# Performance work log

Measured on AMD Instinct MI355X. Metric: run time of the kernel, lower is better.

Reference implementation:

```python
import jax, jax.numpy as jnp
import numpy as np

EPS = 1e-5
NEG_SLOPE = 0.01  # torch LeakyReLU default

def setup_inputs() -> dict:
    N, D, T, H = 4096, 64, 60, 128
    key = jax.random.key(0)
    ks = jax.random.split(key, 12)
    s_ih = 1.0 / np.sqrt(H)
    return {
        "x": jax.random.normal(ks[0], (N, D, T), dtype=jnp.float32),
        "bn1_gamma": jnp.ones((D,), jnp.float32),
        "bn1_beta": jnp.zeros((D,), jnp.float32),
        "W_ih": jax.random.uniform(ks[1], (4 * H, D), jnp.float32, -s_ih, s_ih),
        "W_hh": jax.random.uniform(ks[2], (4 * H, H), jnp.float32, -s_ih, s_ih),
        "b_ih": jax.random.uniform(ks[3], (4 * H,), jnp.float32, -s_ih, s_ih),
        "b_hh": jax.random.uniform(ks[4], (4 * H,), jnp.float32, -s_ih, s_ih),
        "bn2_gamma": jnp.ones((H,), jnp.float32),
        "bn2_beta": jnp.zeros((H,), jnp.float32),
        "W_t": jax.random.uniform(ks[5], (H, H), jnp.float32, -s_ih, s_ih),
        "b_t": jax.random.uniform(ks[6], (H,), jnp.float32, -s_ih, s_ih),
        "a": jax.random.normal(ks[7], (2 * H, 1), dtype=jnp.float32),
        "W_fc": jax.random.uniform(ks[8], (H, H), jnp.float32, -s_ih, s_ih),
        "b_fc": jax.random.uniform(ks[9], (H,), jnp.float32, -s_ih, s_ih),
        "W_out": jax.random.uniform(ks[10], (1, H), jnp.float32, -s_ih, s_ih),
        "b_out": jax.random.uniform(ks[11], (1,), jnp.float32, -s_ih, s_ih),
    }

def _leaky(z):
    return jnp.where(z >= 0, z, NEG_SLOPE * z)

def _lstm_last(x, W_ih, W_hh, b_ih, b_hh):
    # x: [N, T, D] -> last hidden state [N, H]
    N, T, D = x.shape
    H = W_hh.shape[1]
    # precompute input contributions for all timesteps: [T, N, 4H]
    xg = jnp.einsum('ntd,gd->tng', x, W_ih) + b_ih + b_hh
    h0 = jnp.zeros((N, H), x.dtype)
    c0 = jnp.zeros((N, H), x.dtype)
    def step(carry, g):
        h, c = carry
        gates = g + h @ W_hh.T
        i, f, gg, o = jnp.split(gates, 4, axis=-1)
        i = jax.nn.sigmoid(i)
        f = jax.nn.sigmoid(f)
        gg = jnp.tanh(gg)
        o = jax.nn.sigmoid(o)
        c = f * c + i * gg
        h = o * jnp.tanh(c)
        return (h, c), None
    (h, _), _ = jax.lax.scan(step, (h0, c0), xg)
    return h

def reference(x, bn1_gamma, bn1_beta, W_ih, W_hh, b_ih, b_hh,
              bn2_gamma, bn2_beta, W_t, b_t, a, W_fc, b_fc, W_out, b_out):
    # BatchNorm1d over channels of [N, D, T] (training-mode batch stats)
    m1 = x.mean(axis=(0, 2), keepdims=True)
    v1 = x.var(axis=(0, 2), keepdims=True)
    xn = (x - m1) * jax.lax.rsqrt(v1 + EPS)
    xn = xn * bn1_gamma[None, :, None] + bn1_beta[None, :, None]
    xs = jnp.transpose(xn, (0, 2, 1))  # [N, T, D]
    hidden = _lstm_last(xs, W_ih, W_hh, b_ih, b_hh)  # [N, H]
    # BatchNorm1d on [N, H]
    m2 = hidden.mean(axis=0, keepdims=True)
    v2 = hidden.var(axis=0, keepdims=True)
    hidden = (hidden - m2) * jax.lax.rsqrt(v2 + EPS) * bn2_gamma + bn2_beta
    # attention: scores[i,j] = a1.t[j] + a2.t[i]  (decomposed, no NxNx2H concat)
    H = hidden.shape[1]
    t = hidden @ W_t.T + b_t  # [N, H]
    s1 = t @ a[:H, 0]   # contribution of column node j
    s2 = t @ a[H:, 0]   # contribution of row node i
    scores = _leaky(s2[:, None] + s1[None, :])  # [N, N]
    att = jax.nn.softmax(scores, axis=1)
    h2 = att @ hidden + hidden
    h3 = _leaky(h2 @ W_fc.T + b_fc)
    out = jax.nn.sigmoid(h3 @ W_out.T + b_out)  # [N, 1]
    return out.squeeze(-1)
```

## Files before the change

### kernel.cpp

```cpp
#include <hip/hip_runtime.h>
#include <math.h>

constexpr int NN = 4096, DD = 64, TT = 60, HH = 128, GG = 512, KK = 192;

typedef _Float16 h8 __attribute__((ext_vector_type(8)));
typedef float f4 __attribute__((ext_vector_type(4)));

constexpr size_t XNT = 0;
constexpr size_t WFRG = (size_t)TT * NN * DD / 2;
constexpr size_t BSUM = WFRG + 98304 / 2;
constexpr size_t SC1 = BSUM + GG;
constexpr size_t SH1 = SC1 + DD;
constexpr size_t HID = SH1 + DD;
constexpr size_t HBN = HID + (size_t)NN * HH;
constexpr size_t SC2 = HBN + (size_t)NN * HH;
constexpr size_t SH2 = SC2 + HH;
constexpr size_t U1O = SH2 + HH;
constexpr size_t U2O = U1O + HH;
constexpr size_t CCO = U2O + HH;
constexpr size_t S1O = CCO + 4;
constexpr size_t S2O = S1O + NN;
constexpr size_t H2O = S2O + NN;
constexpr size_t SSUM = H2O + (size_t)NN * HH;
constexpr size_t SC16 = SSUM + 392;

__device__ __forceinline__ float fastrcp_(float x) { return __builtin_amdgcn_rcpf(x); }
__device__ __forceinline__ float sigmoidf_(float x) { return fastrcp_(1.f + __expf(-x)); }
__device__ __forceinline__ float tanhfast_(float x) { return 1.f - 2.f * fastrcp_(__expf(2.f * x) + 1.f); }
__device__ __forceinline__ float leakyf_(float z) { return fmaxf(z, 0.01f * z); }

__device__ __forceinline__ unsigned fenc_(float f) {
    unsigned b = __float_as_uint(f);
    return (b & 0x80000000u) ? ~b : (b | 0x80000000u);
}
__device__ __forceinline__ float fdec_(unsigned u) {
    return (u & 0x80000000u) ? __uint_as_float(u & 0x7fffffffu) : __uint_as_float(~u);
}

constexpr int TSTR = 264;

__global__ __launch_bounds__(256) void k_pre(const float* __restrict__ x,
                                             const float* __restrict__ g1,
                                             const float* __restrict__ b1,
                                             const float* __restrict__ Wih,
                                             const float* __restrict__ Whh,
                                             const float* __restrict__ bih,
                                             const float* __restrict__ bhh,
                                             const float* __restrict__ Wt,
                                             const float* __restrict__ bt,
                                             const float* __restrict__ a,
                                             float* __restrict__ ws) {
    int b = blockIdx.x;
    int tid = threadIdx.x;
    if (b >= 1024) {
        if (b == 1408) {
            int k = tid;
            if (k < HH) {
                float u1 = 0.f, u2 = 0.f;
                for (int j = 0; j < HH; j++) {
                    float w = Wt[j * HH + k];
                    u1 = fmaf(w, a[j], u1);
                    u2 = fmaf(w, a[HH + j], u2);
                }
                ws[U1O + k] = u1;
                ws[U2O + k] = u2;
                if (k == 0) {
                    float c1 = 0.f, c2 = 0.f;
                    for (int j = 0; j < HH; j++) {
                        c1 = fmaf(bt[j], a[j], c1);
                        c2 = fmaf(bt[j], a[HH + j], c2);
                    }
                    ws[CCO] = c1;
                    ws[CCO + 1] = c2;
                    ((unsigned*)ws)[CCO + 2] = fenc_(-1e30f);
                }
            }
            return;
        }
        int o = (b - 1024) * 256 + tid;
        _Float16* wf = (_Float16*)(ws + WFRG);
        int j = o & 7;
        int lane = (o >> 3) & 63;
        int rest = o >> 9;
        int ks = rest % 6;
        int gw = rest / 6;
        int g = gw & 3, w = gw >> 2;
        int col = g * 128 + w * 16 + (lane & 15);
        int k = ks * 32 + (lane >> 4) * 8 + j;
        float v = (k < DD) ? Wih[col * DD + k] : Whh[col * HH + (k - DD)];
        wf[o] = (_Float16)v;
        return;
    }
    __shared__ _Float16 stg[TT * TSTR];
    __shared__ float rs[256], rss[256];
    __shared__ float scs[64], shs[64];
    __shared__ unsigned done;
    const float4* xb = (const float4*)(x + (size_t)b * 15360);
#pragma unroll
    for (int q = 0; q < 15; q++) {
        int f = q * 256 + tid;
        float4 v = xb[f];
        int k = f / 15, t0 = (f - k * 15) * 4;
        stg[(t0 + 0) * TSTR + k] = (_Float16)v.x;
        stg[(t0 + 1) * TSTR + k] = (_Float16)v.y;
        stg[(t0 + 2) * TSTR + k] = (_Float16)v.z;
        stg[(t0 + 3) * TSTR + k] = (_Float16)v.w;
    }
    __syncthreads();
    {
        int k = tid;
        float s = 0.f, ss = 0.f;
#pragma unroll
        for (int t = 0; t < TT; t++) {
            float v = (float)stg[t * TSTR + k];
            s += v;
            ss = fmaf(v, v, ss);
        }
        rs[tid] = s; rss[tid] = ss;
    }
    __syncthreads();
    if (tid < 64) {
        float ts = rs[tid] + rs[64 + tid] + rs[128 + tid] + rs[192 + tid];
        float tss = rss[tid] + rss[64 + tid] + rss[128 + tid] + rss[192 + tid];
        atomicAdd(&ws[SSUM + tid], ts);
        atomicAdd(&ws[SSUM + 64 + tid], tss);
    }
    __syncthreads();
    if (tid == 0) {
        __threadfence();
        done = atomicAdd((unsigned*)(ws + SSUM) + 128, 1u);
    }
    __syncthreads();
    _Float16* outp = (_Float16*)ws;
    int n0 = b * 4;
    for (int p = tid; p < 3840; p += 256) {
        int t = p >> 6, i = p & 63;
        *(uint2*)(outp + ((size_t)t * NN + n0) * DD + i * 4) =
            *(const uint2*)(stg + t * TSTR + i * 4);
    }
    if (done != 1023u) return;
    __threadfence();
    if (tid < 64) {
        float cnt = (float)(NN * TT);
        float m = ws[SSUM + tid] / cnt;
        float var = ws[SSUM + 64 + tid] / cnt - m * m;
        float sc = g1[tid] * rsqrtf(var + 1e-5f);
        scs[tid] = sc;
        shs[tid] = b1[tid] - m * sc;
        ((_Float16*)(ws + SC16))[tid] = (_Float16)sc;
    }
    __syncthreads();
    for (int c = tid; c < GG; c += 256) {
        float bsum = bih[c] + bhh[c];
        const float4* wr = (const float4*)(Wih + c * 64);
#pragma unroll
        for (int q = 0; q < 16; q++) {
            float4 wv = wr[q];
            bsum = fmaf(wv.x, shs[q * 4], fmaf(wv.y, shs[q * 4 + 1],
                   fmaf(wv.z, shs[q * 4 + 2], fmaf(wv.w, shs[q * 4 + 3], bsum))));
        }
        ws[BSUM + c] = bsum;
    }
}

__global__ __launch_bounds__(512, 1) void k_lstm(const float* __restrict__ g2,
                                                 const float* __restrict__ b2,
                                                 float* __restrict__ ws) {
    int tid = threadIdx.x;
    int w = tid >> 6, lane = tid & 63;
    int quad = lane >> 4, m = lane & 15;
    int r0 = blockIdx.x * 16;
    __shared__ _Float16 hlds[2][16][136];
    __shared__ unsigned dn;
    const _Float16* wf = (const _Float16*)(ws + WFRG);

    h8 bw[4][6];
#pragma unroll
    for (int g = 0; g < 4; g++)
#pragma unroll
        for (int ks = 0; ks < 6; ks++)
            bw[g][ks] = *(const h8*)(wf + ((((w * 4 + g) * 6 + ks) * 64 + lane) * 8));

    float bias[4];
#pragma unroll
    for (int g = 0; g < 4; g++) bias[g] = ws[BSUM + g * 128 + w * 16 + m];

    const _Float16* sc16 = (const _Float16*)(ws + SC16);
    h8 scv0 = *(const h8*)(sc16 + quad * 8);
    h8 scv1 = *(const h8*)(sc16 + 32 + quad * 8);

    for (int p = tid; p < 2 * 16 * 136; p += 512) ((_Float16*)hlds)[p] = (_Float16)0.f;

    f4 cst = {};
    float hv[4];
    const _Float16* xb = (const _Float16*)ws + (size_t)(r0 + m) * DD + quad * 8;
    __syncthreads();

    h8 ax0 = (*(const h8*)xb) * scv0;
    h8 ax1 = (*(const h8*)(xb + 32)) * scv1;

    for (int t = 0; t < TT; t++) {
        h8 ah[4];
        const _Float16* hb = &hlds[(t + 1) & 1][m][quad * 8];
#pragma unroll
        for (int ks = 0; ks < 4; ks++) ah[ks] = *(const h8*)(hb + ks * 32);
        h8 nx0 = {}, nx1 = {};
        if (t + 1 < TT) {
            const _Float16* xp = xb + (size_t)(t + 1) * NN * DD;
            nx0 = *(const h8*)xp;
            nx1 = *(const h8*)(xp + 32);
        }

        f4 acc[4];
#pragma unroll
        for (int g = 0; g < 4; g++) acc[g] = (f4){bias[g], bias[g], bias[g], bias[g]};
#pragma unroll
        for (int g = 0; g < 4; g++) acc[g] = __builtin_amdgcn_mfma_f32_16x16x32_f16(ax0, bw[g][0], acc[g], 0, 0, 0);
#pragma unroll
        for (int g = 0; g < 4; g++) acc[g] = __builtin_amdgcn_mfma_f32_16x16x32_f16(ax1, bw[g][1], acc[g], 0, 0, 0);
#pragma unroll
        for (int ks = 0; ks < 4; ks++)
#pragma unroll
            for (int g = 0; g < 4; g++)
                acc[g] = __builtin_amdgcn_mfma_f32_16x16x32_f16(ah[ks], bw[g][ks + 2], acc[g], 0, 0, 0);

#pragma unroll
        for (int r = 0; r < 4; r++) {
            float ig = sigmoidf_(acc[0][r]);
            float fg = sigmoidf_(acc[1][r]);
            float gg = tanhfast_(acc[2][r]);
            float og = sigmoidf_(acc[3][r]);
            float c = fmaf(fg, cst[r], ig * gg);
            cst[r] = c;
            hv[r] = og * tanhfast_(c);
        }
        _Float16* wbuf = &hlds[t & 1][0][0];
        int col = w * 16 + m;
#pragma unroll
        for (int r = 0; r < 4; r++) wbuf[(quad * 4 + r) * 136 + col] = (_Float16)hv[r];
        asm volatile("s_waitcnt lgkmcnt(0)\n\ts_barrier" ::: "memory");
        ax0 = nx0 * scv0;
        ax1 = nx1 * scv1;
    }
    int col = w * 16 + m;
#pragma unroll
    for (int r = 0; r < 4; r++)
        ws[HID + (size_t)(r0 + quad * 4 + r) * HH + col] = hv[r];

    float s = hv[0] + hv[1] + hv[2] + hv[3];
    float ss = fmaf(hv[0], hv[0], fmaf(hv[1], hv[1], fmaf(hv[2], hv[2], hv[3] * hv[3])));
    s += __shfl_xor(s, 16, 64); s += __shfl_xor(s, 32, 64);
    ss += __shfl_xor(ss, 16, 64); ss += __shfl_xor(ss, 32, 64);
    if (quad == 0) {
        atomicAdd(&ws[SSUM + 132 + col], s);
        atomicAdd(&ws[SSUM + 260 + col], ss);
    }
    __syncthreads();
    if (tid == 0) {
        __threadfence();
        dn = atomicAdd((unsigned*)(ws + SSUM) + 129, 1u);
    }
    __syncthreads();
    if (dn == 255u) {
        __threadfence();
        if (tid < 128) {
            float mm = ws[SSUM + 132 + tid] / (float)NN;
            float var = ws[SSUM + 260 + tid] / (float)NN - mm * mm;
            float sc = g2[tid] * rsqrtf(var + 1e-5f);
            ws[SC2 + tid] = sc;
            ws[SH2 + tid] = b2[tid] - mm * sc;
        }
    }
}

__global__ void k_hbn(float* __restrict__ ws) {
    __shared__ float sc[HH], sh[HH], u1s[HH], u2s[HH];
    __shared__ _Float16 swz[4096];
    int tid = threadIdx.x;
    if (tid < HH) {
        sc[tid] = ws[SC2 + tid]; sh[tid] = ws[SH2 + tid];
        u1s[tid] = ws[U1O + tid]; u2s[tid] = ws[U2O + tid];
    }
    __syncthreads();
    int r = tid >> 3, l = tid & 7;
    int n = blockIdx.x * 32 + r;
    const float* hr = ws + HID + (size_t)n * HH;
    float* hb = ws + HBN + (size_t)n * HH;
    int lanehi = (r >> 3);
    int jj = r & 7;
    float d1 = 0.f, d2 = 0.f;
    int k0 = l * 16;
#pragma unroll
    for (int q4 = 0; q4 < 4; q4++) {
        float4 hv4 = *(const float4*)&hr[k0 + q4 * 4];
        float4 o;
#pragma unroll
        for (int c = 0; c < 4; c++) {
            int kk = k0 + q4 * 4 + c;
            float v = fmaf(((const float*)&hv4)[c], sc[kk], sh[kk]);
            ((float*)&o)[c] = v;
            swz[l * 512 + (lanehi * 16 + (kk & 15)) * 8 + jj] = (_Float16)v;
            d1 = fmaf(v, u1s[kk], d1);
            d2 = fmaf(v, u2s[kk], d2);
        }
        *(float4*)&hb[k0 + q4 * 4] = o;
    }
#pragma unroll
    for (int o = 1; o < 8; o <<= 1) { d1 += __shfl_xor(d1, o, 64); d2 += __shfl_xor(d2, o, 64); }
    if (l == 0) {
        float s1 = d1 + ws[CCO];
        ws[S1O + n] = s1;
        ws[S2O + n] = d2 + ws[CCO + 1];
        atomicMax((unsigned*)ws + CCO + 2, fenc_(s1));
    }
    __syncthreads();
    _Float16* dst = (_Float16*)ws + (size_t)blockIdx.x * 4096;
    for (int p = tid; p < 512; p += 256)
        *(h8*)(dst + p * 8) = *(const h8*)(swz + p * 8);
}

__global__ __launch_bounds__(512, 1) void k_attfc(const float* __restrict__ Wfc,
                                                  const float* __restrict__ bfc,
                                                  const float* __restrict__ Wout,
                                                  const float* __restrict__ bout,
                                                  float* __restrict__ ws,
                                                  float* __restrict__ out) {
    __shared__ float ls1[NN];
    __shared__ float red[4][16][132];
    __shared__ float psr[4][16];
    __shared__ float h2s[16][132];
    int tid = threadIdx.x;
    int w = tid >> 6, lane = tid & 63;
    int quad = lane >> 4, m = lane & 15;
    int whalf = w >> 2, jsplit = w & 3;
    int n0 = blockIdx.x * 16;
    for (int i = tid; i < NN; i += 512) ls1[i] = ws[S1O + i];
    __syncthreads();
    float s1max = fdec_(((unsigned*)ws)[CCO + 2]);
    float s2n = ws[S2O + n0 + m];
    float mi = leakyf_(s2n + s1max);
    const _Float16* hbsw = (const _Float16*)ws;
    f4 acc[4] = {};
    float psum = 0.f;
    for (int jt0 = 0; jt0 < 32; jt0++) {
        int jt = jsplit * 32 + jt0;
        const float* sp = &ls1[jt * 32 + quad * 8];
        h8 ap;
        float ps = 0.f;
#pragma unroll
        for (int jj = 0; jj < 8; jj++) {
            float z = s2n + sp[jj];
            float p = __expf(leakyf_(z) - mi);
            ps += p;
            ap[jj] = (_Float16)p;
        }
        psum += ps;
#pragma unroll
        for (int hgi = 0; hgi < 4; hgi++) {
            int hg = whalf * 4 + hgi;
            h8 bb = *(const h8*)(hbsw + ((size_t)(jt * 8 + hg) * 64 + lane) * 8);
            acc[hgi] = __builtin_amdgcn_mfma_f32_16x16x32_f16(ap, bb, acc[hgi], 0, 0, 0);
        }
    }
    psum += __shfl_xor(psum, 16, 64);
    psum += __shfl_xor(psum, 32, 64);
    if (whalf == 0 && lane < 16) psr[jsplit][lane] = psum;
#pragma unroll
    for (int hgi = 0; hgi < 4; hgi++) {
        int h = (whalf * 4 + hgi) * 16 + m;
#pragma unroll
        for (int r = 0; r < 4; r++)
            red[jsplit][quad * 4 + r][h] = acc[hgi][r];
    }
    __syncthreads();
    if (tid < 16) {
        float pt = psr[0][tid] + psr[1][tid] + psr[2][tid] + psr[3][tid];
        psr[0][tid] = fastrcp_(pt);
    }
    __syncthreads();
#pragma unroll
    for (int cc = 0; cc < 4; cc++) {
        int c = cc * 512 + tid;
        int row = c >> 7, h = c & 127;
        float v = red[0][row][h] + red[1][row][h] + red[2][row][h] + red[3][row][h];
        h2s[row][h] = fmaf(v, psr[0][row], ws[HBN + (size_t)(n0 + row) * HH + h]);
    }
    __syncthreads();
    int row = tid >> 5, jj = tid & 31;
    float po = 0.f;
#pragma unroll
    for (int q = 0; q < 4; q++) {
        int j = q * 32 + jj;
        const float4* wr = (const float4*)(Wfc + (size_t)j * HH);
        float a = 0.f;
#pragma unroll 8
        for (int kq = 0; kq < 32; kq++) {
            float4 wv = wr[kq];
            float4 hv = *(const float4*)&h2s[row][kq * 4];
            a = fmaf(wv.x, hv.x, fmaf(wv.y, hv.y, fmaf(wv.z, hv.z, fmaf(wv.w, hv.w, a))));
        }
        po = fmaf(leakyf_(a + bfc[j]), Wout[j], po);
    }
#pragma unroll
    for (int o = 1; o < 32; o <<= 1) po += __shfl_xor(po, o, 64);
    if (jj == 0) out[n0 + row] = fastrcp_(1.f + __expf(-(po + bout[0])));
}

extern "C" void kernel_launch(void* const* d_in, const int* in_sizes, int n_in,
                              void* d_out, int out_size, void* d_ws, size_t ws_size,
                              hipStream_t stream) {
    const float* x = (const float*)d_in[0];
    const float* bn1_g = (const float*)d_in[1];
    const float* bn1_b = (const float*)d_in[2];
    const float* W_ih = (const float*)d_in[3];
    const float* W_hh = (const float*)d_in[4];
    const float* b_ih = (const float*)d_in[5];
    const float* b_hh = (const float*)d_in[6];
    const float* bn2_g = (const float*)d_in[7];
    const float* bn2_b = (const float*)d_in[8];
    const float* W_t = (const float*)d_in[9];
    const float* b_t = (const float*)d_in[10];
    const float* a = (const float*)d_in[11];
    const float* W_fc = (const float*)d_in[12];
    const float* b_fc = (const float*)d_in[13];
    const float* W_out = (const float*)d_in[14];
    const float* b_out = (const float*)d_in[15];
    float* ws = (float*)d_ws;
    float* out = (float*)d_out;

    hipMemsetAsync((char*)d_ws + SSUM * sizeof(float), 0, 392 * sizeof(float), stream);
    k_pre<<<1409, 256, 0, stream>>>(x, bn1_g, bn1_b, W_ih, W_hh, b_ih, b_hh, W_t, b_t, a, ws);
    k_lstm<<<NN / 16, 512, 0, stream>>>(bn2_g, bn2_b, ws);
    k_hbn<<<NN / 32, 256, 0, stream>>>(ws);
    k_attfc<<<NN / 16, 512, 0, stream>>>(W_fc, b_fc, W_out, b_out, ws, out);
}
```

Measured before the change: 295.0 us.

## Fold BN1 scale into LSTM weights, split BN atomics, restructure attention waves

The extra k_pre blocks that packed weights and computed the attention vectors are folded into the 1024 main blocks. The BN1 stat atomics are split across two accumulators to reduce contention, and the last block multiplies the packed W_ih fragments by the BN scale. This removes the per-step fp16 multiply of x in the LSTM loop. The attention kernel now gives each of its 8 waves a 16-tile slice of j covering all 128 output columns, reduced through a larger dynamic shared memory buffer. That raises LDS usage and adds a serialized rescale pass in the last k_pre block.

```diff
diff --git a/kernel.cpp b/kernel.cpp
--- a/kernel.cpp
+++ b/kernel.cpp
@@ -52,45 +52,6 @@
                                              float* __restrict__ ws) {
     int b = blockIdx.x;
     int tid = threadIdx.x;
-    if (b >= 1024) {
-        if (b == 1408) {
-            int k = tid;
-            if (k < HH) {
-                float u1 = 0.f, u2 = 0.f;
-                for (int j = 0; j < HH; j++) {
-                    float w = Wt[j * HH + k];
-                    u1 = fmaf(w, a[j], u1);
-                    u2 = fmaf(w, a[HH + j], u2);
-                }
-                ws[U1O + k] = u1;
-                ws[U2O + k] = u2;
-                if (k == 0) {
-                    float c1 = 0.f, c2 = 0.f;
-                    for (int j = 0; j < HH; j++) {
-                        c1 = fmaf(bt[j], a[j], c1);
-                        c2 = fmaf(bt[j], a[HH + j], c2);
-                    }
-                    ws[CCO] = c1;
-                    ws[CCO + 1] = c2;
-                    ((unsigned*)ws)[CCO + 2] = fenc_(-1e30f);
-                }
-            }
-            return;
-        }
-        int o = (b - 1024) * 256 + tid;
-        _Float16* wf = (_Float16*)(ws + WFRG);
-        int j = o & 7;
-        int lane = (o >> 3) & 63;
-        int rest = o >> 9;
-        int ks = rest % 6;
-        int gw = rest / 6;
-        int g = gw & 3, w = gw >> 2;
-        int col = g * 128 + w * 16 + (lane & 15);
-        int k = ks * 32 + (lane >> 4) * 8 + j;
-        float v = (k < DD) ? Wih[col * DD + k] : Whh[col * HH + (k - DD)];
-        wf[o] = (_Float16)v;
-        return;
-    }
     __shared__ _Float16 stg[TT * TSTR];
     __shared__ float rs[256], rss[256];
     __shared__ float scs[64], shs[64];
@@ -122,8 +83,42 @@
     if (tid < 64) {
         float ts = rs[tid] + rs[64 + tid] + rs[128 + tid] + rs[192 + tid];
         float tss = rss[tid] + rss[64 + tid] + rss[128 + tid] + rss[192 + tid];
-        atomicAdd(&ws[SSUM + tid], ts);
-        atomicAdd(&ws[SSUM + 64 + tid], tss);
+        size_t so = (b & 1) ? (SSUM + 132) : SSUM;
+        atomicAdd(&ws[so + tid], ts);
+        atomicAdd(&ws[so + 64 + tid], tss);
+    }
+    if (tid < 96) {
+        int o = b * 96 + tid;
+        _Float16* wf = (_Float16*)(ws + WFRG);
+        int j = o & 7;
+        int lane = (o >> 3) & 63;
+        int rest = o >> 9;
+        int ks = rest % 6;
+        int gw = rest / 6;
+        int col = (gw & 3) * 128 + (gw >> 2) * 16 + (lane & 15);
+        int k = ks * 32 + (lane >> 4) * 8 + j;
+        float v = (k < DD) ? Wih[col * DD + k] : Whh[col * HH + (k - DD)];
+        wf[o] = (_Float16)v;
+    }
+    if (b == 0 && tid < HH) {
+        float u1 = 0.f, u2 = 0.f;
+        for (int j2 = 0; j2 < HH; j2++) {
+            float w0 = Wt[j2 * HH + tid];
+            u1 = fmaf(w0, a[j2], u1);
+            u2 = fmaf(w0, a[HH + j2], u2);
+        }
+        ws[U1O + tid] = u1;
+        ws[U2O + tid] = u2;
+        if (tid == 0) {
+            float c1 = 0.f, c2 = 0.f;
+            for (int j2 = 0; j2 < HH; j2++) {
+                c1 = fmaf(bt[j2], a[j2], c1);
+                c2 = fmaf(bt[j2], a[HH + j2], c2);
+            }
+            ws[CCO] = c1;
+            ws[CCO + 1] = c2;
+            ((unsigned*)ws)[CCO + 2] = fenc_(-1e30f);
+        }
     }
     __syncthreads();
     if (tid == 0) {
@@ -142,14 +137,16 @@
     __threadfence();
     if (tid < 64) {
         float cnt = (float)(NN * TT);
-        float m = ws[SSUM + tid] / cnt;
-        float var = ws[SSUM + 64 + tid] / cnt - m * m;
+        float s_ = ws[SSUM + tid] + ws[SSUM + 132 + tid];
+        float ss_ = ws[SSUM + 64 + tid] + ws[SSUM + 196 + tid];
+        float m = s_ / cnt;
+        float var = ss_ / cnt - m * m;
         float sc = g1[tid] * rsqrtf(var + 1e-5f);
         scs[tid] = sc;
         shs[tid] = b1[tid] - m * sc;
-        ((_Float16*)(ws + SC16))[tid] = (_Float16)sc;
-    }
-    __syncthreads();
+    }
+    __syncthreads();
+    ws[SSUM + 132 + tid] = 0.f;
     for (int c = tid; c < GG; c += 256) {
         float bsum = bih[c] + bhh[c];
         const float4* wr = (const float4*)(Wih + c * 64);
@@ -160,6 +157,16 @@
                    fmaf(wv.z, shs[q * 4 + 2], fmaf(wv.w, shs[q * 4 + 3], bsum))));
         }
         ws[BSUM + c] = bsum;
+    }
+    {
+        _Float16* wfm = (_Float16*)(ws + WFRG);
+        for (int o = tid; o < 32768; o += 256) {
+            int j = o & 7, lane = (o >> 3) & 63, rest = o >> 9;
+            int ks = rest & 1;
+            int k = ks * 32 + (lane >> 4) * 8 + j;
+            size_t off = ((size_t)(rest >> 1) * 6 + ks) * 512 + (size_t)lane * 8 + j;
+            wfm[off] = (_Float16)((float)wfm[off] * scs[k]);
+        }
     }
 }
 
@@ -185,10 +192,6 @@
 #pragma unroll
     for (int g = 0; g < 4; g++) bias[g] = ws[BSUM + g * 128 + w * 16 + m];
 
-    const _Float16* sc16 = (const _Float16*)(ws + SC16);
-    h8 scv0 = *(const h8*)(sc16 + quad * 8);
-    h8 scv1 = *(const h8*)(sc16 + 32 + quad * 8);
-
     for (int p = tid; p < 2 * 16 * 136; p += 512) ((_Float16*)hlds)[p] = (_Float16)0.f;
 
     f4 cst = {};
@@ -196,8 +199,8 @@
     const _Float16* xb = (const _Float16*)ws + (size_t)(r0 + m) * DD + quad * 8;
     __syncthreads();
 
-    h8 ax0 = (*(const h8*)xb) * scv0;
-    h8 ax1 = (*(const h8*)(xb + 32)) * scv1;
+    h8 ax0 = *(const h8*)xb;
+    h8 ax1 = *(const h8*)(xb + 32);
 
     for (int t = 0; t < TT; t++) {
         h8 ah[4];
@@ -239,8 +242,8 @@
 #pragma unroll
         for (int r = 0; r < 4; r++) wbuf[(quad * 4 + r) * 136 + col] = (_Float16)hv[r];
         asm volatile("s_waitcnt lgkmcnt(0)\n\ts_barrier" ::: "memory");
-        ax0 = nx0 * scv0;
-        ax1 = nx1 * scv1;
+        ax0 = nx0;
+        ax1 = nx1;
     }
     int col = w * 16 + m;
 #pragma unroll
@@ -325,14 +328,14 @@
                                                   const float* __restrict__ bout,
                                                   float* __restrict__ ws,
                                                   float* __restrict__ out) {
-    __shared__ float ls1[NN];
-    __shared__ float red[4][16][132];
-    __shared__ float psr[4][16];
-    __shared__ float h2s[16][132];
+    extern __shared__ float dyn[];
+    float* ls1 = dyn;
+    float* red = dyn + 4096;
+    float* psr = red + 16896;
+    float* h2s = psr + 128;
     int tid = threadIdx.x;
     int w = tid >> 6, lane = tid & 63;
     int quad = lane >> 4, m = lane & 15;
-    int whalf = w >> 2, jsplit = w & 3;
     int n0 = blockIdx.x * 16;
     for (int i = tid; i < NN; i += 512) ls1[i] = ws[S1O + i];
     __syncthreads();
@@ -340,10 +343,10 @@
     float s2n = ws[S2O + n0 + m];
     float mi = leakyf_(s2n + s1max);
     const _Float16* hbsw = (const _Float16*)ws;
-    f4 acc[4] = {};
+    f4 acc[8] = {};
     float psum = 0.f;
-    for (int jt0 = 0; jt0 < 32; jt0++) {
-        int jt = jsplit * 32 + jt0;
+    for (int jt0 = 0; jt0 < 16; jt0++) {
+        int jt = w * 16 + jt0;
         const float* sp = &ls1[jt * 32 + quad * 8];
         h8 ap;
         float ps = 0.f;
@@ -356,34 +359,37 @@
         }
         psum += ps;
 #pragma unroll
-        for (int hgi = 0; hgi < 4; hgi++) {
-            int hg = whalf * 4 + hgi;
+        for (int hg = 0; hg < 8; hg++) {
             h8 bb = *(const h8*)(hbsw + ((size_t)(jt * 8 + hg) * 64 + lane) * 8);
-            acc[hgi] = __builtin_amdgcn_mfma_f32_16x16x32_f16(ap, bb, acc[hgi], 0, 0, 0);
+            acc[hg] = __builtin_amdgcn_mfma_f32_16x16x32_f16(ap, bb, acc[hg], 0, 0, 0);
         }
     }
     psum += __shfl_xor(psum, 16, 64);
     psum += __shfl_xor(psum, 32, 64);
-    if (whalf == 0 && lane < 16) psr[jsplit][lane] = psum;
-#pragma unroll
-    for (int hgi = 0; hgi < 4; hgi++) {
-        int h = (whalf * 4 + hgi) * 16 + m;
+    if (lane < 16) psr[w * 16 + lane] = psum;
+#pragma unroll
+    for (int hg = 0; hg < 8; hg++) {
+        int h = hg * 16 + m;
 #pragma unroll
         for (int r = 0; r < 4; r++)
-            red[jsplit][quad * 4 + r][h] = acc[hgi][r];
+            red[(w * 16 + quad * 4 + r) * 132 + h] = acc[hg][r];
     }
     __syncthreads();
     if (tid < 16) {
-        float pt = psr[0][tid] + psr[1][tid] + psr[2][tid] + psr[3][tid];
-        psr[0][tid] = fastrcp_(pt);
+        float pt = 0.f;
+#pragma unroll
+        for (int s = 0; s < 8; s++) pt += psr[s * 16 + tid];
+        psr[tid] = fastrcp_(pt);
     }
     __syncthreads();
 #pragma unroll
     for (int cc = 0; cc < 4; cc++) {
         int c = cc * 512 + tid;
         int row = c >> 7, h = c & 127;
-        float v = red[0][row][h] + red[1][row][h] + red[2][row][h] + red[3][row][h];
-        h2s[row][h] = fmaf(v, psr[0][row], ws[HBN + (size_t)(n0 + row) * HH + h]);
+        float v = 0.f;
+#pragma unroll
+        for (int s = 0; s < 8; s++) v += red[(s * 16 + row) * 132 + h];
+        h2s[row * 132 + h] = fmaf(v, psr[row], ws[HBN + (size_t)(n0 + row) * HH + h]);
     }
     __syncthreads();
     int row = tid >> 5, jj = tid & 31;
@@ -396,7 +402,7 @@
 #pragma unroll 8
         for (int kq = 0; kq < 32; kq++) {
             float4 wv = wr[kq];
-            float4 hv = *(const float4*)&h2s[row][kq * 4];
+            float4 hv = *(const float4*)&h2s[row * 132 + kq * 4];
             a = fmaf(wv.x, hv.x, fmaf(wv.y, hv.y, fmaf(wv.z, hv.z, fmaf(wv.w, hv.w, a))));
         }
         po = fmaf(leakyf_(a + bfc[j]), Wout[j], po);
@@ -428,9 +434,16 @@
     float* ws = (float*)d_ws;
     float* out = (float*)d_out;
 
+    static bool attr_set = false;
+    if (!attr_set) {
+        hipFuncSetAttribute((const void*)k_attfc,
+                            hipFuncAttributeMaxDynamicSharedMemorySize, 92928);
+        attr_set = true;
+    }
+
     hipMemsetAsync((char*)d_ws + SSUM * sizeof(float), 0, 392 * sizeof(float), stream);
-    k_pre<<<1409, 256, 0, stream>>>(x, bn1_g, bn1_b, W_ih, W_hh, b_ih, b_hh, W_t, b_t, a, ws);
+    k_pre<<<1024, 256, 0, stream>>>(x, bn1_g, bn1_b, W_ih, W_hh, b_ih, b_hh, W_t, b_t, a, ws);
     k_lstm<<<NN / 16, 512, 0, stream>>>(bn2_g, bn2_b, ws);
     k_hbn<<<NN / 32, 256, 0, stream>>>(ws);
-    k_attfc<<<NN / 16, 512, 0, stream>>>(W_fc, b_fc, W_out, b_out, ws, out);
-}
+    k_attfc<<<NN / 16, 512, 92928, stream>>>(W_fc, b_fc, W_out, b_out, ws, out);
+}
```

Result: slower. 327.5 us (+11.0%).
